# Kernel tuning notes

Hardware: AMD Instinct MI355X
Metric: run time of the kernel (lower is better)

## Reference

```python
import jax, jax.numpy as jnp
import numpy as np

IN_F = 1024
OUT_F = 1024
INT_DIM = 128


def setup_inputs() -> dict:
    key = jax.random.key(0)
    k_x, k_wc, k_bc, k_pw, k_pb = jax.random.split(key, 5)
    # coef init per init_kaiming_uniform: fan_in = in_features, gain for
    # leaky_relu(a=sqrt(5)) = sqrt(2/(1+5)) = sqrt(1/3)
    fan_in = IN_F
    gain = np.sqrt(2.0 / (1.0 + 5.0))
    out_std = gain / np.sqrt(fan_in)
    w_bound = np.sqrt(3.0) * np.sqrt(3.0 / INT_DIM) * out_std
    b_bound = w_bound  # same int_dim and out_std for bias coef
    x = jax.random.normal(k_x, (8, 2048, IN_F), dtype=jnp.float32)
    weight_coef = jax.random.uniform(k_wc, (INT_DIM,), jnp.float32, -w_bound, w_bound)
    bias_coef = jax.random.uniform(k_bc, (INT_DIM,), jnp.float32, -b_bound, b_bound)
    # fixed (seed-determined, non-learned) random projection bases
    P_w = jax.random.normal(k_pw, (INT_DIM, OUT_F * IN_F), dtype=jnp.float32)
    P_b = jax.random.normal(k_pb, (INT_DIM, OUT_F), dtype=jnp.float32)
    return {"x": x, "weight_coef": weight_coef, "bias_coef": bias_coef,
            "P_w": P_w, "P_b": P_b}


def reference(x, weight_coef, bias_coef, P_w, P_b):
    # Expand low-dim coefs through the fixed random projection into the
    # full weight/bias (RandumbTensor materialization), then F.linear.
    W = (weight_coef @ P_w).reshape(OUT_F, IN_F)   # [out, in]
    b = bias_coef @ P_b                            # [out]
    # y = x A^T + b
    return jnp.einsum('bsi,oi->bso', x, W) + b
```

## Files before the change

kernel.cpp:

```cpp
#include <hip/hip_runtime.h>
#include <stdint.h>

#define IN_F 1024
#define OUT_F 1024
#define INT_DIM 128
#define M_ROWS 16384

#define BM 128
#define BN 128
#define BK 32

typedef float f32x4 __attribute__((ext_vector_type(4)));
typedef __bf16 bf16x8 __attribute__((ext_vector_type(8)));

__device__ __forceinline__ unsigned short f2bf(float f) {
  unsigned int u = __float_as_uint(f);
  u += 0x7fffu + ((u >> 16) & 1u);
  return (unsigned short)(u >> 16);
}

__device__ __forceinline__ void async_copy16(void* lds_dst, const void* gsrc) {
  __builtin_amdgcn_global_load_lds(
      (const __attribute__((address_space(1))) void*)gsrc,
      (__attribute__((address_space(3))) void*)lds_dst, 16, 0, 0);
}

__global__ void expand_w_kernel(const float* __restrict__ coef,
                                const float* __restrict__ Pw,
                                unsigned short* __restrict__ W) {
  __shared__ float c[INT_DIM];
  if (threadIdx.x < INT_DIM) c[threadIdx.x] = coef[threadIdx.x];
  __syncthreads();
  const int j4 = blockIdx.x * 256 + threadIdx.x;
  const float4* P4 = (const float4*)Pw;
  float4 acc = make_float4(0.f, 0.f, 0.f, 0.f);
#pragma unroll 8
  for (int d = 0; d < INT_DIM; ++d) {
    float4 p = P4[(size_t)d * (OUT_F * IN_F / 4) + j4];
    float cd = c[d];
    acc.x += cd * p.x;
    acc.y += cd * p.y;
    acc.z += cd * p.z;
    acc.w += cd * p.w;
  }
  union { unsigned short us[4]; uint2 u; } o;
  o.us[0] = f2bf(acc.x);
  o.us[1] = f2bf(acc.y);
  o.us[2] = f2bf(acc.z);
  o.us[3] = f2bf(acc.w);
  ((uint2*)W)[j4] = o.u;
}

__global__ void expand_b_kernel(const float* __restrict__ coef,
                                const float* __restrict__ Pb,
                                float* __restrict__ bias) {
  const int o = blockIdx.x * 256 + threadIdx.x;
  float acc = 0.f;
#pragma unroll 8
  for (int d = 0; d < INT_DIM; ++d) acc += coef[d] * Pb[d * OUT_F + o];
  bias[o] = acc;
}

__global__ void cvt_x_kernel(const float4* __restrict__ x,
                             uint2* __restrict__ xb) {
  const int i = blockIdx.x * 256 + threadIdx.x;
  float4 v = x[i];
  union { unsigned short us[4]; uint2 u; } o;
  o.us[0] = f2bf(v.x);
  o.us[1] = f2bf(v.y);
  o.us[2] = f2bf(v.z);
  o.us[3] = f2bf(v.w);
  xb[i] = o.u;
}

__global__ __launch_bounds__(256) void gemm_bt_kernel(
    const unsigned short* __restrict__ A,
    const unsigned short* __restrict__ B,
    const float* __restrict__ bias,
    float* __restrict__ C) {
  constexpr int K = IN_F;
  constexpr int N = OUT_F;
  __shared__ unsigned short sA[BM * BK];
  __shared__ unsigned short sB[BN * BK];

  const int tid = threadIdx.x;
  const int bm = blockIdx.y * BM;
  const int bn = blockIdx.x * BN;
  const int lane = tid & 63;
  const int wave = tid >> 6;
  const int wm = (wave >> 1) * 64;
  const int wn = (wave & 1) * 64;
  const int lm = lane & 15;
  const int quad = lane >> 4;

  const int q0 = tid;
  const int q1 = tid + 256;
  const int r0 = q0 >> 2, kc0 = (q0 & 3) * 8;
  const int r1 = q1 >> 2, kc1 = (q1 & 3) * 8;

  f32x4 acc[4][4];
  const f32x4 zero = {0.f, 0.f, 0.f, 0.f};
#pragma unroll
  for (int i = 0; i < 4; ++i)
#pragma unroll
    for (int j = 0; j < 4; ++j) acc[i][j] = zero;

  for (int k0 = 0; k0 < K; k0 += BK) {
    async_copy16(&sA[q0 * 8], &A[(size_t)(bm + r0) * K + k0 + kc0]);
    async_copy16(&sA[q1 * 8], &A[(size_t)(bm + r1) * K + k0 + kc1]);
    async_copy16(&sB[q0 * 8], &B[(size_t)(bn + r0) * K + k0 + kc0]);
    async_copy16(&sB[q1 * 8], &B[(size_t)(bn + r1) * K + k0 + kc1]);
    __syncthreads();

    bf16x8 af[4], bf[4];
#pragma unroll
    for (int f = 0; f < 4; ++f)
      af[f] = *(const bf16x8*)&sA[(wm + f * 16 + lm) * BK + quad * 8];
#pragma unroll
    for (int f = 0; f < 4; ++f)
      bf[f] = *(const bf16x8*)&sB[(wn + f * 16 + lm) * BK + quad * 8];

#pragma unroll
    for (int fm = 0; fm < 4; ++fm)
#pragma unroll
      for (int fn = 0; fn < 4; ++fn)
        acc[fm][fn] = __builtin_amdgcn_mfma_f32_16x16x32_bf16(
            af[fm], bf[fn], acc[fm][fn], 0, 0, 0);
    __syncthreads();
  }

  float bv[4];
#pragma unroll
  for (int fn = 0; fn < 4; ++fn) bv[fn] = bias[bn + wn + fn * 16 + lm];
#pragma unroll
  for (int fm = 0; fm < 4; ++fm) {
#pragma unroll
    for (int r = 0; r < 4; ++r) {
      const int row = bm + wm + fm * 16 + quad * 4 + r;
      float* crow = C + (size_t)row * N + bn + wn + lm;
#pragma unroll
      for (int fn = 0; fn < 4; ++fn) crow[fn * 16] = acc[fm][fn][r] + bv[fn];
    }
  }
}

extern "C" void kernel_launch(void* const* d_in, const int* in_sizes, int n_in,
                              void* d_out, int out_size, void* d_ws,
                              size_t ws_size, hipStream_t stream) {
  const float* x = (const float*)d_in[0];
  const float* wc = (const float*)d_in[1];
  const float* bc = (const float*)d_in[2];
  const float* Pw = (const float*)d_in[3];
  const float* Pb = (const float*)d_in[4];
  float* out = (float*)d_out;

  unsigned short* W = (unsigned short*)d_ws;
  float* bias = (float*)((char*)d_ws + (2u << 20));
  unsigned short* xb = (unsigned short*)((char*)d_ws + (4u << 20));

  expand_w_kernel<<<OUT_F * IN_F / 4 / 256, 256, 0, stream>>>(wc, Pw, W);
  expand_b_kernel<<<OUT_F / 256, 256, 0, stream>>>(bc, Pb, bias);
  cvt_x_kernel<<<(M_ROWS * IN_F / 4) / 256, 256, 0, stream>>>(
      (const float4*)x, (uint2*)xb);

  dim3 grid(OUT_F / BN, M_ROWS / BM);
  gemm_bt_kernel<<<grid, 256, 0, stream>>>(xb, W, bias, out);
}
```

Baseline: 815.0 us.

## Fuse x fp32-to-bf16 conversion into GEMM via swizzled fp32 LDS tiles

Removes the separate x conversion kernel. The GEMM now loads fp32 x tiles straight into LDS using an XOR-swizzled layout and converts them to bf16 in registers before the MFMA. This saves a full write and read of a bf16 copy of x, about 64 MB of traffic. The cost is that every N-tile block rereads fp32 A, which is twice the bytes of the bf16 copy, and LDS use and conversion ALU work go up. The grid order is also swapped so that blocks sharing the same M rows run at different times, which may change how much of A is reused in L2.

```diff
diff --git a/kernel.cpp b/kernel.cpp
--- a/kernel.cpp
+++ b/kernel.cpp
@@ -61,31 +61,19 @@
   bias[o] = acc;
 }
 
-__global__ void cvt_x_kernel(const float4* __restrict__ x,
-                             uint2* __restrict__ xb) {
-  const int i = blockIdx.x * 256 + threadIdx.x;
-  float4 v = x[i];
-  union { unsigned short us[4]; uint2 u; } o;
-  o.us[0] = f2bf(v.x);
-  o.us[1] = f2bf(v.y);
-  o.us[2] = f2bf(v.z);
-  o.us[3] = f2bf(v.w);
-  xb[i] = o.u;
-}
-
-__global__ __launch_bounds__(256) void gemm_bt_kernel(
-    const unsigned short* __restrict__ A,
+__global__ __launch_bounds__(256) void gemm_xf32_bt_kernel(
+    const float* __restrict__ A,
     const unsigned short* __restrict__ B,
     const float* __restrict__ bias,
     float* __restrict__ C) {
   constexpr int K = IN_F;
   constexpr int N = OUT_F;
-  __shared__ unsigned short sA[BM * BK];
+  __shared__ float sA[BM * BK];
   __shared__ unsigned short sB[BN * BK];
 
   const int tid = threadIdx.x;
-  const int bm = blockIdx.y * BM;
-  const int bn = blockIdx.x * BN;
+  const int bm = blockIdx.x * BM;
+  const int bn = blockIdx.y * BN;
   const int lane = tid & 63;
   const int wave = tid >> 6;
   const int wm = (wave >> 1) * 64;
@@ -93,10 +81,23 @@
   const int lm = lane & 15;
   const int quad = lane >> 4;
 
+  const float* aSrc[4];
+#pragma unroll
+  for (int j = 0; j < 4; ++j) {
+    const int d = tid + 256 * j;
+    const int rd = d >> 3;
+    const int cd = d & 7;
+    aSrc[j] = A + (size_t)(bm + rd) * K + ((cd ^ (rd & 7)) << 2);
+  }
+
   const int q0 = tid;
   const int q1 = tid + 256;
   const int r0 = q0 >> 2, kc0 = (q0 & 3) * 8;
   const int r1 = q1 >> 2, kc1 = (q1 & 3) * 8;
+
+  const int sw = lm & 7;
+  const int co0 = (((quad << 1) | 0) ^ sw) << 2;
+  const int co1 = (((quad << 1) | 1) ^ sw) << 2;
 
   f32x4 acc[4][4];
   const f32x4 zero = {0.f, 0.f, 0.f, 0.f};
@@ -106,26 +107,36 @@
     for (int j = 0; j < 4; ++j) acc[i][j] = zero;
 
   for (int k0 = 0; k0 < K; k0 += BK) {
-    async_copy16(&sA[q0 * 8], &A[(size_t)(bm + r0) * K + k0 + kc0]);
-    async_copy16(&sA[q1 * 8], &A[(size_t)(bm + r1) * K + k0 + kc1]);
+#pragma unroll
+    for (int j = 0; j < 4; ++j)
+      async_copy16(&sA[(tid + 256 * j) * 4], aSrc[j] + k0);
     async_copy16(&sB[q0 * 8], &B[(size_t)(bn + r0) * K + k0 + kc0]);
     async_copy16(&sB[q1 * 8], &B[(size_t)(bn + r1) * K + k0 + kc1]);
     __syncthreads();
 
-    bf16x8 af[4], bf[4];
+    bf16x8 af[4], bfr[4];
+#pragma unroll
+    for (int f = 0; f < 4; ++f) {
+      const int rbase = (wm + f * 16 + lm) * BK;
+      const f32x4 lo = *(const f32x4*)&sA[rbase + co0];
+      const f32x4 hi = *(const f32x4*)&sA[rbase + co1];
+      bf16x8 v;
+      v[0] = (__bf16)lo[0]; v[1] = (__bf16)lo[1];
+      v[2] = (__bf16)lo[2]; v[3] = (__bf16)lo[3];
+      v[4] = (__bf16)hi[0]; v[5] = (__bf16)hi[1];
+      v[6] = (__bf16)hi[2]; v[7] = (__bf16)hi[3];
+      af[f] = v;
+    }
 #pragma unroll
     for (int f = 0; f < 4; ++f)
-      af[f] = *(const bf16x8*)&sA[(wm + f * 16 + lm) * BK + quad * 8];
-#pragma unroll
-    for (int f = 0; f < 4; ++f)
-      bf[f] = *(const bf16x8*)&sB[(wn + f * 16 + lm) * BK + quad * 8];
+      bfr[f] = *(const bf16x8*)&sB[(wn + f * 16 + lm) * BK + quad * 8];
 
 #pragma unroll
     for (int fm = 0; fm < 4; ++fm)
 #pragma unroll
       for (int fn = 0; fn < 4; ++fn)
         acc[fm][fn] = __builtin_amdgcn_mfma_f32_16x16x32_bf16(
-            af[fm], bf[fn], acc[fm][fn], 0, 0, 0);
+            af[fm], bfr[fn], acc[fm][fn], 0, 0, 0);
     __syncthreads();
   }
 
@@ -156,13 +167,10 @@
 
   unsigned short* W = (unsigned short*)d_ws;
   float* bias = (float*)((char*)d_ws + (2u << 20));
-  unsigned short* xb = (unsigned short*)((char*)d_ws + (4u << 20));
 
   expand_w_kernel<<<OUT_F * IN_F / 4 / 256, 256, 0, stream>>>(wc, Pw, W);
   expand_b_kernel<<<OUT_F / 256, 256, 0, stream>>>(bc, Pb, bias);
-  cvt_x_kernel<<<(M_ROWS * IN_F / 4) / 256, 256, 0, stream>>>(
-      (const float4*)x, (uint2*)xb);
 
-  dim3 grid(OUT_F / BN, M_ROWS / BM);
-  gemm_bt_kernel<<<grid, 256, 0, stream>>>(xb, W, bias, out);
+  dim3 grid(M_ROWS / BM, OUT_F / BN);
+  gemm_xf32_bt_kernel<<<grid, 256, 0, stream>>>(x, W, bias, out);
 }
```

New measurement: 808.0 us. Within noise of the previous version (-0.9%).
